# Performance work log

Hardware: AMD Instinct MI355X
Metric: run time of the kernel (lower is better)

Reference implementation:

```python
import jax, jax.numpy as jnp
import numpy as np

N = 4096
STEPS = 100


def setup_inputs() -> dict:
    key = jax.random.key(0)
    k1, k2 = jax.random.split(key)
    z = jax.random.normal(k1, (N, 2), dtype=jnp.float32) * 0.1  # points in the disc
    K = jax.random.normal(k2, (N, N), dtype=jnp.float32) * 0.1  # coupling matrix param
    omega = jnp.float32(0.1)  # learned natural frequency (scalar)
    dt = jnp.float32(0.05)
    return {"z": z, "K": K, "omega": omega, "dt": dt, "steps": STEPS}


def reference(z, K, omega, dt, steps):
    n = z.shape[0]
    inv2n = 1.0 / (2.0 * n)
    z_c = jax.lax.complex(z[:, 0], z[:, 1])          # (N,) complex64
    K_c = K.astype(jnp.complex64)                    # (N,N) complex (zero imag part)

    def step(zc, _):
        S = K_c @ jnp.conj(zc)                       # (N,)
        T = K_c @ zc                                 # (N,)
        dz = -inv2n * S * zc**2 + omega * zc + inv2n * T
        zc = zc + dt * dz
        a = jnp.abs(zc)
        mask = a >= 0.999
        safe_a = jnp.where(mask, a, 1.0)             # avoid div-by-zero in untaken branch
        zc = jnp.where(mask, zc / safe_a * 0.999, zc)
        return zc, None

    z_c, _ = jax.lax.scan(step, z_c, None, length=steps)

    z_final = jnp.stack([jnp.real(z_c), jnp.imag(z_c)], axis=1)  # (N,2)
    norms = jnp.linalg.norm(z_final, axis=1, keepdims=True)
    mask = norms >= 0.999
    safe_n = jnp.where(mask, norms, 1.0)
    z_final = jnp.where(mask, z_final / safe_n * 0.999, z_final)
    return z_final
```

## Files before the change

kernel.cpp:

```cpp
#include <hip/hip_runtime.h>

#define NN 4096
#define NSTEPS 100
#define TPB 512
#define NBLK 256

__device__ __forceinline__ void zstore_u64(float2* p, unsigned long long u) {
    __hip_atomic_store((unsigned long long*)p, u, __ATOMIC_RELAXED,
                       __HIP_MEMORY_SCOPE_AGENT);
}
__device__ __forceinline__ unsigned long long zload_u64(const float2* p) {
    return __hip_atomic_load((const unsigned long long*)p, __ATOMIC_RELAXED,
                             __HIP_MEMORY_SCOPE_AGENT);
}

__global__ __launch_bounds__(TPB, 2) void k_persist(
    const float* __restrict__ K, const float2* __restrict__ z0,
    float2* __restrict__ zb0, float2* __restrict__ zb1,
    float2* __restrict__ zfinal, const float* __restrict__ omega_p,
    const float* __restrict__ dt_p) {
    __shared__ float P[2][8][64];

    const int tid  = threadIdx.x;
    const int bid  = blockIdx.x;
    const int w    = tid >> 6, lane = tid & 63;
    const int colbase = w * 512 + lane;

    const float omega = *omega_p;
    const float dt    = *dt_p;
    const float inv2n = 1.0f / (2.0f * NN);

    float kA[16][8];
#pragma unroll
    for (int r = 0; r < 16; ++r) {
        const float* Kr = K + (size_t)(bid * 16 + r) * NN + colbase;
#pragma unroll
        for (int j = 0; j < 8; ++j) kA[r][j] = Kr[j * 64];
    }

    float x = 0.f, y = 0.f;
    if (w == 0 && lane < 16) {
        float2 zc = z0[bid * 16 + lane];
        x = zc.x; y = zc.y;
    }

    for (int s = 0; s < NSTEPS; ++s) {
#pragma unroll
        for (int r = 0; r < 16; ++r)
#pragma unroll
            for (int j = 0; j < 8; ++j) asm volatile("" : "+v"(kA[r][j]));

        float zre[8], zim[8];
        if (s == 0) {
#pragma unroll
            for (int j = 0; j < 8; ++j) {
                float2 zc = z0[colbase + j * 64];
                zre[j] = zc.x; zim[j] = zc.y;
            }
        } else {
            const float2* zsrc = (s & 1) ? zb1 : zb0;
            const unsigned tag = (unsigned)(s & 7);
            unsigned long long v[8];
#pragma unroll
            for (int j = 0; j < 8; ++j)
                v[j] = zload_u64(zsrc + colbase + j * 64);
            unsigned stale = 0u;
#pragma unroll
            for (int j = 0; j < 8; ++j)
                stale |= (((unsigned)v[j] & 7u) != tag) ? (1u << j) : 0u;
            while (stale) {
                __builtin_amdgcn_s_sleep(1);
#pragma unroll
                for (int j = 0; j < 8; ++j)
                    if (stale & (1u << j))
                        v[j] = zload_u64(zsrc + colbase + j * 64);
#pragma unroll
                for (int j = 0; j < 8; ++j)
                    if ((stale & (1u << j)) && ((unsigned)v[j] & 7u) == tag)
                        stale &= ~(1u << j);
            }
#pragma unroll
            for (int j = 0; j < 8; ++j) {
                union { unsigned u; float f; } cx, cy;
                cx.u = (unsigned)v[j];
                cy.u = (unsigned)(v[j] >> 32);
                zre[j] = cx.f; zim[j] = cy.f;
            }
        }

        float sr[16], si[16];
#pragma unroll
        for (int r = 0; r < 16; ++r) { sr[r] = 0.f; si[r] = 0.f; }
#pragma unroll
        for (int j = 0; j < 8; ++j) {
#pragma unroll
            for (int r = 0; r < 16; ++r) {
                sr[r] += kA[r][j] * zre[j];
                si[r] += kA[r][j] * zim[j];
            }
        }

        float a32[32];
#pragma unroll
        for (int r = 0; r < 16; ++r) { a32[r] = sr[r]; a32[16 + r] = si[r]; }
        float b16[16];
#pragma unroll
        for (int m = 0; m < 16; ++m) {
            float aa = a32[2 * m], bb = a32[2 * m + 1];
            bool hi = lane & 1;
            float snd = hi ? aa : bb, kp = hi ? bb : aa;
            b16[m] = kp + __shfl_xor(snd, 1, 64);
        }
        float b8[8];
#pragma unroll
        for (int m = 0; m < 8; ++m) {
            float aa = b16[2 * m], bb = b16[2 * m + 1];
            bool hi = lane & 2;
            float snd = hi ? aa : bb, kp = hi ? bb : aa;
            b8[m] = kp + __shfl_xor(snd, 2, 64);
        }
        float b4[4];
#pragma unroll
        for (int m = 0; m < 4; ++m) {
            float aa = b8[2 * m], bb = b8[2 * m + 1];
            bool hi = lane & 4;
            float snd = hi ? aa : bb, kp = hi ? bb : aa;
            b4[m] = kp + __shfl_xor(snd, 4, 64);
        }
        float b2[2];
#pragma unroll
        for (int m = 0; m < 2; ++m) {
            float aa = b4[2 * m], bb = b4[2 * m + 1];
            bool hi = lane & 8;
            float snd = hi ? aa : bb, kp = hi ? bb : aa;
            b2[m] = kp + __shfl_xor(snd, 8, 64);
        }
        {
            float aa = b2[0], bb = b2[1];
            bool hi = lane & 16;
            float snd = hi ? aa : bb, kp = hi ? bb : aa;
            float red = kp + __shfl_xor(snd, 16, 64);
            P[s & 1][w][lane] = red;
        }
        __syncthreads();

        if (w == 0 && lane < 16) {
            const int par = s & 1;
            float u = 0.f, vv = 0.f;
#pragma unroll
            for (int q = 0; q < 8; ++q) {
                u  += P[par][q][lane]      + P[par][q][32 + lane];
                vv += P[par][q][16 + lane] + P[par][q][48 + lane];
            }
            float A = x * x - y * y;
            float B = 2.0f * x * y;
            float dzr = inv2n * (u  - (u * A + vv * B)) + omega * x;
            float dzi = inv2n * (vv - (u * B - vv * A)) + omega * y;
            float nx = x + dt * dzr;
            float ny = y + dt * dzi;
            float a2 = nx * nx + ny * ny;
            if (a2 >= 0.999f * 0.999f) {
                float sc = 0.999f / sqrtf(a2);
                nx *= sc; ny *= sc;
            }
            x = nx; y = ny;
            int gr = bid * 16 + lane;
            if (s == NSTEPS - 1) {
                zfinal[gr] = make_float2(nx, ny);
            } else {
                union { float f; unsigned u; } cx, cy;
                cx.f = nx; cy.f = ny;
                cx.u = (cx.u & ~7u) | (unsigned)((s + 1) & 7);
                unsigned long long pk =
                    (unsigned long long)cx.u |
                    ((unsigned long long)cy.u << 32);
                float2* zo = ((s + 1) & 1) ? zb1 : zb0;
                zstore_u64(zo + gr, pk);
            }
        }
    }
}

__global__ __launch_bounds__(256) void k_step_f32(
    const float* __restrict__ K, const float2* __restrict__ zin,
    float2* __restrict__ zout, const float* __restrict__ omega_p,
    const float* __restrict__ dt_p, int n) {
    const int wave = threadIdx.x >> 6;
    const int lane = threadIdx.x & 63;
    const int row  = blockIdx.x * 4 + wave;
    if (row >= n) return;
    float sr = 0.0f, si = 0.0f;
    for (int c = lane; c < n; c += 64) {
        float k = K[(size_t)row * n + c];
        float2 z = zin[c];
        sr += k * z.x;
        si += k * z.y;
    }
#pragma unroll
    for (int off = 32; off; off >>= 1) {
        sr += __shfl_down(sr, off, 64);
        si += __shfl_down(si, off, 64);
    }
    if (lane == 0) {
        float u = sr, v = si;
        float2 zc = zin[row];
        float x = zc.x, y = zc.y;
        float inv2n = 1.0f / (2.0f * n);
        float A = x * x - y * y, B = 2.0f * x * y;
        float dzr = inv2n * (u - (u * A + v * B)) + (*omega_p) * x;
        float dzi = inv2n * (v - (u * B - v * A)) + (*omega_p) * y;
        float nx = x + (*dt_p) * dzr, ny = y + (*dt_p) * dzi;
        float a2 = nx * nx + ny * ny;
        if (a2 >= 0.999f * 0.999f) { float sc = 0.999f / sqrtf(a2); nx *= sc; ny *= sc; }
        zout[row] = make_float2(nx, ny);
    }
}

extern "C" void kernel_launch(void* const* d_in, const int* in_sizes, int n_in,
                              void* d_out, int out_size, void* d_ws, size_t ws_size,
                              hipStream_t stream) {
    const float2* z0      = (const float2*)d_in[0];
    const float*  K       = (const float*)d_in[1];
    const float*  omega_p = (const float*)d_in[2];
    const float*  dt_p    = (const float*)d_in[3];
    const int n = in_sizes[0] / 2;
    float2* out = (float2*)d_out;

    const size_t need = 2 * (size_t)NN * sizeof(float2);
    if (n == NN && ws_size >= need) {
        float2* zb0 = (float2*)d_ws;
        float2* zb1 = zb0 + NN;
        hipMemsetAsync(d_ws, 0, need, stream);
        k_persist<<<NBLK, TPB, 0, stream>>>(K, z0, zb0, zb1, out,
                                            omega_p, dt_p);
    } else {
        float2* zb0 = (float2*)d_ws;
        float2* zb1 = zb0 + n;
        const float2* cur = z0;
        for (int s = 0; s < NSTEPS; ++s) {
            float2* nxt = (s == NSTEPS - 1) ? out : ((s & 1) ? zb1 : zb0);
            k_step_f32<<<(n + 3) / 4, 256, 0, stream>>>(K, cur, nxt, omega_p, dt_p, n);
            cur = nxt;
        }
    }
}
```

Baseline: 457.8 us.

## Spread row finalize across all waves and issue next-step z loads early

```diff
diff --git a/kernel.cpp b/kernel.cpp
--- a/kernel.cpp
+++ b/kernel.cpp
@@ -19,7 +19,7 @@
     float2* __restrict__ zb0, float2* __restrict__ zb1,
     float2* __restrict__ zfinal, const float* __restrict__ omega_p,
     const float* __restrict__ dt_p) {
-    __shared__ float P[2][8][64];
+    __shared__ float P[2][8][68];
 
     const int tid  = threadIdx.x;
     const int bid  = blockIdx.x;
@@ -39,10 +39,12 @@
     }
 
     float x = 0.f, y = 0.f;
-    if (w == 0 && lane < 16) {
-        float2 zc = z0[bid * 16 + lane];
+    if ((lane & 31) == 0) {
+        float2 zc = z0[bid * 16 + 2 * w + (lane >> 5)];
         x = zc.x; y = zc.y;
     }
+
+    unsigned long long v[8];
 
     for (int s = 0; s < NSTEPS; ++s) {
 #pragma unroll
@@ -60,10 +62,6 @@
         } else {
             const float2* zsrc = (s & 1) ? zb1 : zb0;
             const unsigned tag = (unsigned)(s & 7);
-            unsigned long long v[8];
-#pragma unroll
-            for (int j = 0; j < 8; ++j)
-                v[j] = zload_u64(zsrc + colbase + j * 64);
             unsigned stale = 0u;
 #pragma unroll
             for (int j = 0; j < 8; ++j)
@@ -100,6 +98,13 @@
             }
         }
 
+        if (s + 1 < NSTEPS) {
+            const float2* zn = ((s + 1) & 1) ? zb1 : zb0;
+#pragma unroll
+            for (int j = 0; j < 8; ++j)
+                v[j] = zload_u64(zn + colbase + j * 64);
+        }
+
         float a32[32];
 #pragma unroll
         for (int r = 0; r < 16; ++r) { a32[r] = sr[r]; a32[16 + r] = si[r]; }
@@ -144,38 +149,48 @@
         }
         __syncthreads();
 
-        if (w == 0 && lane < 16) {
+        {
             const int par = s & 1;
-            float u = 0.f, vv = 0.f;
-#pragma unroll
-            for (int q = 0; q < 8; ++q) {
-                u  += P[par][q][lane]      + P[par][q][32 + lane];
-                vv += P[par][q][16 + lane] + P[par][q][48 + lane];
-            }
-            float A = x * x - y * y;
-            float B = 2.0f * x * y;
-            float dzr = inv2n * (u  - (u * A + vv * B)) + omega * x;
-            float dzi = inv2n * (vv - (u * B - vv * A)) + omega * y;
-            float nx = x + dt * dzr;
-            float ny = y + dt * dzi;
-            float a2 = nx * nx + ny * ny;
-            if (a2 >= 0.999f * 0.999f) {
-                float sc = 0.999f / sqrtf(a2);
-                nx *= sc; ny *= sc;
-            }
-            x = nx; y = ny;
-            int gr = bid * 16 + lane;
-            if (s == NSTEPS - 1) {
-                zfinal[gr] = make_float2(nx, ny);
-            } else {
-                union { float f; unsigned u; } cx, cy;
-                cx.f = nx; cy.f = ny;
-                cx.u = (cx.u & ~7u) | (unsigned)((s + 1) & 7);
-                unsigned long long pk =
-                    (unsigned long long)cx.u |
-                    ((unsigned long long)cy.u << 32);
-                float2* zo = ((s + 1) & 1) ? zb1 : zb0;
-                zstore_u64(zo + gr, pk);
+            const int r0 = 2 * w, r1 = 2 * w + 1;
+            int q    = lane & 7;
+            int half = (lane >> 3) & 1;
+            int sel  = lane >> 4;
+            int rr   = (sel & 2) ? r1 : r0;
+            int idx  = ((sel & 1) << 4) + rr;
+            float val = P[par][q][half * 32 + idx];
+            val += __shfl_xor(val, 1, 64);
+            val += __shfl_xor(val, 2, 64);
+            val += __shfl_xor(val, 4, 64);
+            val += __shfl_xor(val, 8, 64);
+            float other = __shfl_xor(val, 16, 64);
+            if ((lane & 31) == 0) {
+                float u  = val;
+                float vv = other;
+                float A = x * x - y * y;
+                float B = 2.0f * x * y;
+                float dzr = inv2n * (u  - (u * A + vv * B)) + omega * x;
+                float dzi = inv2n * (vv - (u * B - vv * A)) + omega * y;
+                float nx = x + dt * dzr;
+                float ny = y + dt * dzi;
+                float a2 = nx * nx + ny * ny;
+                if (a2 >= 0.999f * 0.999f) {
+                    float sc = 0.999f / sqrtf(a2);
+                    nx *= sc; ny *= sc;
+                }
+                x = nx; y = ny;
+                int gr = bid * 16 + r0 + (lane >> 5);
+                if (s == NSTEPS - 1) {
+                    zfinal[gr] = make_float2(nx, ny);
+                } else {
+                    union { float f; unsigned u; } cx, cy;
+                    cx.f = nx; cy.f = ny;
+                    cx.u = (cx.u & ~7u) | (unsigned)((s + 1) & 7);
+                    unsigned long long pk =
+                        (unsigned long long)cx.u |
+                        ((unsigned long long)cy.u << 32);
+                    float2* zo = ((s + 1) & 1) ? zb1 : zb0;
+                    zstore_u64(zo + gr, pk);
+                }
             }
         }
     }
```

New measurement: 392.6 us. -14.2%, faster.
